# Kernel tuning notes

Measured on AMD Instinct MI355X. Metric: run time of the kernel, lower is better.

The kernel has to match this reference:

```python
import jax, jax.numpy as jnp
import numpy as np

IN_FEATURES = 100000
OUT_FEATURES = 100000
NNZ = 1600000
BATCH = 64


def setup_inputs() -> dict:
    key = jax.random.key(0)
    k1, k2, k3, k4, k5 = jax.random.split(key, 5)
    x = jax.random.normal(k1, (BATCH, IN_FEATURES), dtype=jnp.float32)
    values = jax.random.normal(k2, (NNZ,), dtype=jnp.float32)
    bias = jax.random.normal(k3, (OUT_FEATURES,), dtype=jnp.float32)
    # torch COO is coalesced -> row indices sorted (rows = dst of transposed matrix)
    rows = jnp.sort(jax.random.randint(k4, (NNZ,), 0, OUT_FEATURES, dtype=jnp.int64))
    cols = jax.random.randint(k5, (NNZ,), 0, IN_FEATURES, dtype=jnp.int64)
    return {"x": x, "values": values, "bias": bias, "rows": rows, "cols": cols}


def reference(x, values, bias, rows, cols):
    # out = x @ conn  <=>  out.T = conn_T @ x.T, conn_T given in COO (rows=dst, cols=src)
    # gather source activations along edges: (nnz, B)
    contrib = x[:, cols].T * values[:, None]
    # scatter-add into destinations: (out_features, B)
    out_t = jax.ops.segment_sum(contrib, rows, num_segments=OUT_FEATURES,
                                indices_are_sorted=True)
    return out_t.T + bias  # (B, out_features)
```

## Files before the change

### kernel.cpp

```cpp
#include <hip/hip_runtime.h>
#include <hip/hip_fp16.h>

#define IN_F   100000
#define OUT_F  100000
#define NNZ_N  1600000
#define TC     256
#define TBLK   ((IN_F + TC - 1) / TC)
#define SBLK   ((NNZ_N + 255) / 256)

__device__ __forceinline__ float2 h2f(unsigned u) {
    const __half2 h = *reinterpret_cast<const __half2*>(&u);
    return __half22float2(h);
}

__global__ __launch_bounds__(256) void k_prep(
    const float* __restrict__ x,
    const int*   __restrict__ rows,
    const int*   __restrict__ cols,
    const float* __restrict__ vals,
    unsigned* __restrict__ xh,
    int*      __restrict__ rstart,
    uint2*    __restrict__ pairs) {
    __shared__ unsigned tile[TC][33];
    const int bid = blockIdx.x;
    const int t   = threadIdx.x;

    if (bid < TBLK) {
        const int i0   = bid * TC;
        const int colr = i0 + t;
        if (colr < IN_F) {
            #pragma unroll 8
            for (int p = 0; p < 32; ++p) {
                const float a = x[(size_t)(2 * p)     * IN_F + colr];
                const float b = x[(size_t)(2 * p + 1) * IN_F + colr];
                const __half2 h = __floats2half2_rn(a, b);
                tile[t][p] = *reinterpret_cast<const unsigned*>(&h);
            }
        }
        __syncthreads();
        const int u  = t & 31;
        const int c8 = t >> 5;
        for (int cc = c8; cc < TC; cc += 8) {
            const int col = i0 + cc;
            if (col < IN_F)
                xh[(size_t)col * 32 + u] = tile[cc][u];
        }
    } else {
        const int e = (bid - TBLK) * 256 + t;
        if (e >= NNZ_N) return;
        const int cur  = rows[e];
        const int prev = (e == 0) ? -1 : rows[e - 1];
        for (int r = prev + 1; r <= cur; ++r) rstart[r] = e;
        if (e == NNZ_N - 1)
            for (int r = cur + 1; r <= OUT_F; ++r) rstart[r] = NNZ_N;
        pairs[e] = make_uint2((unsigned)cols[e], __float_as_uint(vals[e]));
    }
}

__global__ __launch_bounds__(512, 4) void k_spmm(
    const uint4* __restrict__ xh4,
    const uint2* __restrict__ pairs,
    const int*   __restrict__ rstart_g,
    const float* __restrict__ bias,
    float* __restrict__ out) {
    __shared__ int   rs[65];
    __shared__ float tile[64][65];
    const int r0   = blockIdx.x * 64;
    const int t    = threadIdx.x;
    const int lane = t & 63;
    const int w    = t >> 6;

    if (t < 65) {
        int idx = r0 + t; if (idx > OUT_F) idx = OUT_F;
        rs[t] = rstart_g[idx];
    }
    __syncthreads();

    const int g   = lane >> 3;
    const int sub = lane & 7;
    const int lj  = (w << 3) + g;
    const int s   = rs[lj];
    const int e   = rs[lj + 1];

    float acc[8];
    #pragma unroll
    for (int i = 0; i < 8; ++i) acc[i] = 0.f;

    for (int base = s; base < e; base += 4) {
        const int e1 = e - 1;
        const int i1 = (base + 1 < e) ? base + 1 : e1;
        const int i2 = (base + 2 < e) ? base + 2 : e1;
        const int i3 = (base + 3 < e) ? base + 3 : e1;
        const uint2 p0 = pairs[base];
        const uint2 p1 = pairs[i1];
        const uint2 p2 = pairs[i2];
        const uint2 p3 = pairs[i3];
        const float v0 = __uint_as_float(p0.y);
        const float v1 = (base + 1 < e) ? __uint_as_float(p1.y) : 0.f;
        const float v2 = (base + 2 < e) ? __uint_as_float(p2.y) : 0.f;
        const float v3 = (base + 3 < e) ? __uint_as_float(p3.y) : 0.f;
        const uint4 u0 = xh4[(size_t)p0.x * 8 + sub];
        const uint4 u1 = xh4[(size_t)p1.x * 8 + sub];
        const uint4 u2 = xh4[(size_t)p2.x * 8 + sub];
        const uint4 u3 = xh4[(size_t)p3.x * 8 + sub];
        float2 f;
        f = h2f(u0.x); acc[0] = fmaf(v0, f.x, acc[0]); acc[1] = fmaf(v0, f.y, acc[1]);
        f = h2f(u0.y); acc[2] = fmaf(v0, f.x, acc[2]); acc[3] = fmaf(v0, f.y, acc[3]);
        f = h2f(u0.z); acc[4] = fmaf(v0, f.x, acc[4]); acc[5] = fmaf(v0, f.y, acc[5]);
        f = h2f(u0.w); acc[6] = fmaf(v0, f.x, acc[6]); acc[7] = fmaf(v0, f.y, acc[7]);
        f = h2f(u1.x); acc[0] = fmaf(v1, f.x, acc[0]); acc[1] = fmaf(v1, f.y, acc[1]);
        f = h2f(u1.y); acc[2] = fmaf(v1, f.x, acc[2]); acc[3] = fmaf(v1, f.y, acc[3]);
        f = h2f(u1.z); acc[4] = fmaf(v1, f.x, acc[4]); acc[5] = fmaf(v1, f.y, acc[5]);
        f = h2f(u1.w); acc[6] = fmaf(v1, f.x, acc[6]); acc[7] = fmaf(v1, f.y, acc[7]);
        f = h2f(u2.x); acc[0] = fmaf(v2, f.x, acc[0]); acc[1] = fmaf(v2, f.y, acc[1]);
        f = h2f(u2.y); acc[2] = fmaf(v2, f.x, acc[2]); acc[3] = fmaf(v2, f.y, acc[3]);
        f = h2f(u2.z); acc[4] = fmaf(v2, f.x, acc[4]); acc[5] = fmaf(v2, f.y, acc[5]);
        f = h2f(u2.w); acc[6] = fmaf(v2, f.x, acc[6]); acc[7] = fmaf(v2, f.y, acc[7]);
        f = h2f(u3.x); acc[0] = fmaf(v3, f.x, acc[0]); acc[1] = fmaf(v3, f.y, acc[1]);
        f = h2f(u3.y); acc[2] = fmaf(v3, f.x, acc[2]); acc[3] = fmaf(v3, f.y, acc[3]);
        f = h2f(u3.z); acc[4] = fmaf(v3, f.x, acc[4]); acc[5] = fmaf(v3, f.y, acc[5]);
        f = h2f(u3.w); acc[6] = fmaf(v3, f.x, acc[6]); acc[7] = fmaf(v3, f.y, acc[7]);
    }

    #pragma unroll
    for (int i = 0; i < 8; ++i) tile[lj][(sub << 3) + i] = acc[i];
    __syncthreads();

    const int rc = r0 + lane;
    if (rc < OUT_F) {
        const float bv = bias[rc];
        for (int bb = w; bb < 64; bb += 8)
            out[(size_t)bb * OUT_F + rc] = tile[lane][bb] + bv;
    }
}

__global__ __launch_bounds__(256) void k_spmm_fallback(
    const float* __restrict__ x,
    const float* __restrict__ vals,
    const int*   __restrict__ rows,
    const int*   __restrict__ cols,
    const float* __restrict__ bias,
    float* __restrict__ out) {
    __shared__ int   rstart[65];
    __shared__ float tile[64][65];
    const int r0   = blockIdx.x * 64;
    const int t    = threadIdx.x;
    const int lane = t & 63;
    const int w    = t >> 6;
    if (t < 65) {
        const int target = r0 + t;
        int lo = 0, hi = NNZ_N;
        while (lo < hi) {
            const int mid = (lo + hi) >> 1;
            if (rows[mid] < target) lo = mid + 1; else hi = mid;
        }
        rstart[t] = lo;
    }
    __syncthreads();
    for (int j = w; j < 64; j += 4) {
        const int s = rstart[j], e = rstart[j + 1];
        float acc = 0.f;
        const size_t base = (size_t)lane * IN_F;
        for (int idx = s; idx < e; ++idx)
            acc = fmaf(vals[idx], x[base + cols[idx]], acc);
        tile[j][lane] = acc;
    }
    __syncthreads();
    const int c = lane;
    if (r0 + c < OUT_F) {
        const float bv = bias[r0 + c];
        for (int bb = w; bb < 64; bb += 4)
            out[(size_t)bb * OUT_F + (r0 + c)] = tile[c][bb] + bv;
    }
}

extern "C" void kernel_launch(void* const* d_in, const int* in_sizes, int n_in,
                              void* d_out, int out_size, void* d_ws, size_t ws_size,
                              hipStream_t stream) {
    const float* x      = (const float*)d_in[0];
    const float* values = (const float*)d_in[1];
    const float* bias   = (const float*)d_in[2];
    const int*   rows   = (const int*)d_in[3];
    const int*   cols   = (const int*)d_in[4];
    float*       out    = (float*)d_out;

    const size_t xh_bytes = (size_t)IN_F * 32 * sizeof(unsigned);
    const size_t rs_off   = (xh_bytes + 255) & ~(size_t)255;
    const size_t rs_bytes = (size_t)(OUT_F + 1) * sizeof(int);
    const size_t pr_off   = (rs_off + rs_bytes + 255) & ~(size_t)255;
    const size_t need     = pr_off + (size_t)NNZ_N * sizeof(uint2);

    const int row_blocks = (OUT_F + 63) / 64;

    if (ws_size >= need) {
        unsigned* xh     = (unsigned*)d_ws;
        int*      rstart = (int*)((char*)d_ws + rs_off);
        uint2*    pairs  = (uint2*)((char*)d_ws + pr_off);
        k_prep<<<TBLK + SBLK, 256, 0, stream>>>(x, rows, cols, values, xh, rstart, pairs);
        k_spmm<<<row_blocks, 512, 0, stream>>>(
            (const uint4*)xh, pairs, rstart, bias, out);
    } else {
        k_spmm_fallback<<<row_blocks, 256, 0, stream>>>(x, values, rows, cols, bias, out);
    }
}
```

Baseline: 132.6 us.

## Bin nonzeros by column chunk per row block to improve gather cache locality

```diff
diff --git a/kernel.cpp b/kernel.cpp
--- a/kernel.cpp
+++ b/kernel.cpp
@@ -6,7 +6,9 @@
 #define NNZ_N  1600000
 #define TC     256
 #define TBLK   ((IN_F + TC - 1) / TC)
-#define SBLK   ((NNZ_N + 255) / 256)
+#define RBLK   ((OUT_F + 63) / 64)
+#define NCH    4
+#define CHW    25000
 
 __device__ __forceinline__ float2 h2f(unsigned u) {
     const __half2 h = *reinterpret_cast<const __half2*>(&u);
@@ -19,9 +21,12 @@
     const int*   __restrict__ cols,
     const float* __restrict__ vals,
     unsigned* __restrict__ xh,
-    int*      __restrict__ rstart,
-    uint2*    __restrict__ pairs) {
+    uint2*    __restrict__ pairs,
+    int*      __restrict__ cs) {
     __shared__ unsigned tile[TC][33];
+    __shared__ int hist[256];
+    __shared__ int off[256];
+    __shared__ int sb[2];
     const int bid = blockIdx.x;
     const int t   = threadIdx.x;
 
@@ -46,87 +51,121 @@
                 xh[(size_t)col * 32 + u] = tile[cc][u];
         }
     } else {
-        const int e = (bid - TBLK) * 256 + t;
-        if (e >= NNZ_N) return;
-        const int cur  = rows[e];
-        const int prev = (e == 0) ? -1 : rows[e - 1];
-        for (int r = prev + 1; r <= cur; ++r) rstart[r] = e;
-        if (e == NNZ_N - 1)
-            for (int r = cur + 1; r <= OUT_F; ++r) rstart[r] = NNZ_N;
-        pairs[e] = make_uint2((unsigned)cols[e], __float_as_uint(vals[e]));
+        const int b  = bid - TBLK;
+        const int r0 = b * 64;
+        if (t < 2) {
+            const int target = r0 + t * 64;
+            int lo = 0, hi = NNZ_N;
+            while (lo < hi) {
+                const int mid = (lo + hi) >> 1;
+                if (rows[mid] < target) lo = mid + 1; else hi = mid;
+            }
+            sb[t] = lo;
+        }
+        hist[t] = 0;
+        __syncthreads();
+        const int s = sb[0], e = sb[1];
+        for (int i = s + t; i < e; i += 256)
+            atomicAdd(&hist[(cols[i] / CHW) * 64 + (rows[i] - r0)], 1);
+        __syncthreads();
+        if (t < 64) {
+            const int s0 = hist[4 * t + 0];
+            const int s1 = hist[4 * t + 1];
+            const int s2 = hist[4 * t + 2];
+            const int s3 = hist[4 * t + 3];
+            const int tot = s0 + s1 + s2 + s3;
+            int sc = tot;
+            #pragma unroll
+            for (int d = 1; d < 64; d <<= 1) {
+                const int n = __shfl_up(sc, d);
+                if (t >= d) sc += n;
+            }
+            int base = s + (sc - tot);
+            off[4 * t + 0] = base; cs[(size_t)b * 257 + 4 * t + 0] = base; base += s0;
+            off[4 * t + 1] = base; cs[(size_t)b * 257 + 4 * t + 1] = base; base += s1;
+            off[4 * t + 2] = base; cs[(size_t)b * 257 + 4 * t + 2] = base; base += s2;
+            off[4 * t + 3] = base; cs[(size_t)b * 257 + 4 * t + 3] = base; base += s3;
+        }
+        if (t == 0) cs[(size_t)b * 257 + 256] = e;
+        __syncthreads();
+        for (int i = s + t; i < e; i += 256) {
+            const int c   = cols[i];
+            const int bin = (c / CHW) * 64 + (rows[i] - r0);
+            const int pos = atomicAdd(&off[bin], 1);
+            pairs[pos] = make_uint2((unsigned)c, __float_as_uint(vals[i]));
+        }
     }
 }
 
 __global__ __launch_bounds__(512, 4) void k_spmm(
     const uint4* __restrict__ xh4,
     const uint2* __restrict__ pairs,
-    const int*   __restrict__ rstart_g,
+    const int*   __restrict__ cs,
     const float* __restrict__ bias,
     float* __restrict__ out) {
-    __shared__ int   rs[65];
+    __shared__ int   rs[257];
     __shared__ float tile[64][65];
-    const int r0   = blockIdx.x * 64;
+    const int b    = blockIdx.x;
     const int t    = threadIdx.x;
     const int lane = t & 63;
     const int w    = t >> 6;
-
-    if (t < 65) {
-        int idx = r0 + t; if (idx > OUT_F) idx = OUT_F;
-        rs[t] = rstart_g[idx];
-    }
-    __syncthreads();
-
-    const int g   = lane >> 3;
-    const int sub = lane & 7;
-    const int lj  = (w << 3) + g;
-    const int s   = rs[lj];
-    const int e   = rs[lj + 1];
+    const int g    = t >> 3;
+    const int sub  = t & 7;
+
+    if (t < 257) rs[t] = cs[(size_t)b * 257 + t];
+    __syncthreads();
 
     float acc[8];
     #pragma unroll
     for (int i = 0; i < 8; ++i) acc[i] = 0.f;
 
-    for (int base = s; base < e; base += 4) {
-        const int e1 = e - 1;
-        const int i1 = (base + 1 < e) ? base + 1 : e1;
-        const int i2 = (base + 2 < e) ? base + 2 : e1;
-        const int i3 = (base + 3 < e) ? base + 3 : e1;
-        const uint2 p0 = pairs[base];
-        const uint2 p1 = pairs[i1];
-        const uint2 p2 = pairs[i2];
-        const uint2 p3 = pairs[i3];
-        const float v0 = __uint_as_float(p0.y);
-        const float v1 = (base + 1 < e) ? __uint_as_float(p1.y) : 0.f;
-        const float v2 = (base + 2 < e) ? __uint_as_float(p2.y) : 0.f;
-        const float v3 = (base + 3 < e) ? __uint_as_float(p3.y) : 0.f;
-        const uint4 u0 = xh4[(size_t)p0.x * 8 + sub];
-        const uint4 u1 = xh4[(size_t)p1.x * 8 + sub];
-        const uint4 u2 = xh4[(size_t)p2.x * 8 + sub];
-        const uint4 u3 = xh4[(size_t)p3.x * 8 + sub];
-        float2 f;
-        f = h2f(u0.x); acc[0] = fmaf(v0, f.x, acc[0]); acc[1] = fmaf(v0, f.y, acc[1]);
-        f = h2f(u0.y); acc[2] = fmaf(v0, f.x, acc[2]); acc[3] = fmaf(v0, f.y, acc[3]);
-        f = h2f(u0.z); acc[4] = fmaf(v0, f.x, acc[4]); acc[5] = fmaf(v0, f.y, acc[5]);
-        f = h2f(u0.w); acc[6] = fmaf(v0, f.x, acc[6]); acc[7] = fmaf(v0, f.y, acc[7]);
-        f = h2f(u1.x); acc[0] = fmaf(v1, f.x, acc[0]); acc[1] = fmaf(v1, f.y, acc[1]);
-        f = h2f(u1.y); acc[2] = fmaf(v1, f.x, acc[2]); acc[3] = fmaf(v1, f.y, acc[3]);
-        f = h2f(u1.z); acc[4] = fmaf(v1, f.x, acc[4]); acc[5] = fmaf(v1, f.y, acc[5]);
-        f = h2f(u1.w); acc[6] = fmaf(v1, f.x, acc[6]); acc[7] = fmaf(v1, f.y, acc[7]);
-        f = h2f(u2.x); acc[0] = fmaf(v2, f.x, acc[0]); acc[1] = fmaf(v2, f.y, acc[1]);
-        f = h2f(u2.y); acc[2] = fmaf(v2, f.x, acc[2]); acc[3] = fmaf(v2, f.y, acc[3]);
-        f = h2f(u2.z); acc[4] = fmaf(v2, f.x, acc[4]); acc[5] = fmaf(v2, f.y, acc[5]);
-        f = h2f(u2.w); acc[6] = fmaf(v2, f.x, acc[6]); acc[7] = fmaf(v2, f.y, acc[7]);
-        f = h2f(u3.x); acc[0] = fmaf(v3, f.x, acc[0]); acc[1] = fmaf(v3, f.y, acc[1]);
-        f = h2f(u3.y); acc[2] = fmaf(v3, f.x, acc[2]); acc[3] = fmaf(v3, f.y, acc[3]);
-        f = h2f(u3.z); acc[4] = fmaf(v3, f.x, acc[4]); acc[5] = fmaf(v3, f.y, acc[5]);
-        f = h2f(u3.w); acc[6] = fmaf(v3, f.x, acc[6]); acc[7] = fmaf(v3, f.y, acc[7]);
-    }
-
     #pragma unroll
-    for (int i = 0; i < 8; ++i) tile[lj][(sub << 3) + i] = acc[i];
-    __syncthreads();
-
-    const int rc = r0 + lane;
+    for (int k = 0; k < NCH; ++k) {
+        const int s = rs[k * 64 + g];
+        const int e = rs[k * 64 + g + 1];
+        for (int base = s; base < e; base += 4) {
+            const int e1 = e - 1;
+            const int i1 = (base + 1 < e) ? base + 1 : e1;
+            const int i2 = (base + 2 < e) ? base + 2 : e1;
+            const int i3 = (base + 3 < e) ? base + 3 : e1;
+            const uint2 p0 = pairs[base];
+            const uint2 p1 = pairs[i1];
+            const uint2 p2 = pairs[i2];
+            const uint2 p3 = pairs[i3];
+            const float v0 = __uint_as_float(p0.y);
+            const float v1 = (base + 1 < e) ? __uint_as_float(p1.y) : 0.f;
+            const float v2 = (base + 2 < e) ? __uint_as_float(p2.y) : 0.f;
+            const float v3 = (base + 3 < e) ? __uint_as_float(p3.y) : 0.f;
+            const uint4 u0 = xh4[(size_t)p0.x * 8 + sub];
+            const uint4 u1 = xh4[(size_t)p1.x * 8 + sub];
+            const uint4 u2 = xh4[(size_t)p2.x * 8 + sub];
+            const uint4 u3 = xh4[(size_t)p3.x * 8 + sub];
+            float2 f;
+            f = h2f(u0.x); acc[0] = fmaf(v0, f.x, acc[0]); acc[1] = fmaf(v0, f.y, acc[1]);
+            f = h2f(u0.y); acc[2] = fmaf(v0, f.x, acc[2]); acc[3] = fmaf(v0, f.y, acc[3]);
+            f = h2f(u0.z); acc[4] = fmaf(v0, f.x, acc[4]); acc[5] = fmaf(v0, f.y, acc[5]);
+            f = h2f(u0.w); acc[6] = fmaf(v0, f.x, acc[6]); acc[7] = fmaf(v0, f.y, acc[7]);
+            f = h2f(u1.x); acc[0] = fmaf(v1, f.x, acc[0]); acc[1] = fmaf(v1, f.y, acc[1]);
+            f = h2f(u1.y); acc[2] = fmaf(v1, f.x, acc[2]); acc[3] = fmaf(v1, f.y, acc[3]);
+            f = h2f(u1.z); acc[4] = fmaf(v1, f.x, acc[4]); acc[5] = fmaf(v1, f.y, acc[5]);
+            f = h2f(u1.w); acc[6] = fmaf(v1, f.x, acc[6]); acc[7] = fmaf(v1, f.y, acc[7]);
+            f = h2f(u2.x); acc[0] = fmaf(v2, f.x, acc[0]); acc[1] = fmaf(v2, f.y, acc[1]);
+            f = h2f(u2.y); acc[2] = fmaf(v2, f.x, acc[2]); acc[3] = fmaf(v2, f.y, acc[3]);
+            f = h2f(u2.z); acc[4] = fmaf(v2, f.x, acc[4]); acc[5] = fmaf(v2, f.y, acc[5]);
+            f = h2f(u2.w); acc[6] = fmaf(v2, f.x, acc[6]); acc[7] = fmaf(v2, f.y, acc[7]);
+            f = h2f(u3.x); acc[0] = fmaf(v3, f.x, acc[0]); acc[1] = fmaf(v3, f.y, acc[1]);
+            f = h2f(u3.y); acc[2] = fmaf(v3, f.x, acc[2]); acc[3] = fmaf(v3, f.y, acc[3]);
+            f = h2f(u3.z); acc[4] = fmaf(v3, f.x, acc[4]); acc[5] = fmaf(v3, f.y, acc[5]);
+            f = h2f(u3.w); acc[6] = fmaf(v3, f.x, acc[6]); acc[7] = fmaf(v3, f.y, acc[7]);
+        }
+        __syncthreads();
+    }
+
+    #pragma unroll
+    for (int i = 0; i < 8; ++i) tile[g][(sub << 3) + i] = acc[i];
+    __syncthreads();
+
+    const int rc = b * 64 + lane;
     if (rc < OUT_F) {
         const float bv = bias[rc];
         for (int bb = w; bb < 64; bb += 8)
@@ -185,21 +224,18 @@
     float*       out    = (float*)d_out;
 
     const size_t xh_bytes = (size_t)IN_F * 32 * sizeof(unsigned);
-    const size_t rs_off   = (xh_bytes + 255) & ~(size_t)255;
-    const size_t rs_bytes = (size_t)(OUT_F + 1) * sizeof(int);
-    const size_t pr_off   = (rs_off + rs_bytes + 255) & ~(size_t)255;
-    const size_t need     = pr_off + (size_t)NNZ_N * sizeof(uint2);
-
-    const int row_blocks = (OUT_F + 63) / 64;
+    const size_t pr_off   = (xh_bytes + 255) & ~(size_t)255;
+    const size_t pr_bytes = (size_t)NNZ_N * sizeof(uint2);
+    const size_t cb_off   = (pr_off + pr_bytes + 255) & ~(size_t)255;
+    const size_t need     = cb_off + (size_t)RBLK * 257 * sizeof(int);
 
     if (ws_size >= need) {
-        unsigned* xh     = (unsigned*)d_ws;
-        int*      rstart = (int*)((char*)d_ws + rs_off);
-        uint2*    pairs  = (uint2*)((char*)d_ws + pr_off);
-        k_prep<<<TBLK + SBLK, 256, 0, stream>>>(x, rows, cols, values, xh, rstart, pairs);
-        k_spmm<<<row_blocks, 512, 0, stream>>>(
-            (const uint4*)xh, pairs, rstart, bias, out);
+        unsigned* xh    = (unsigned*)d_ws;
+        uint2*    pairs = (uint2*)((char*)d_ws + pr_off);
+        int*      cs    = (int*)((char*)d_ws + cb_off);
+        k_prep<<<TBLK + RBLK, 256, 0, stream>>>(x, rows, cols, values, xh, pairs, cs);
+        k_spmm<<<RBLK, 512, 0, stream>>>((const uint4*)xh, pairs, cs, bias, out);
     } else {
-        k_spmm_fallback<<<row_blocks, 256, 0, stream>>>(x, values, rows, cols, bias, out);
-    }
-}
+        k_spmm_fallback<<<RBLK, 256, 0, stream>>>(x, values, rows, cols, bias, out);
+    }
+}
```

After: 149.1 us. +12.5%, slower.

## Drop pairs/rstart preprocessing; binary-search row starts and read cols/vals directly

Applied to the files above, without the earlier changes.

```diff
diff --git a/kernel.cpp b/kernel.cpp
--- a/kernel.cpp
+++ b/kernel.cpp
@@ -6,61 +6,44 @@
 #define NNZ_N  1600000
 #define TC     256
 #define TBLK   ((IN_F + TC - 1) / TC)
-#define SBLK   ((NNZ_N + 255) / 256)
+#define RBLK   ((OUT_F + 63) / 64)
 
 __device__ __forceinline__ float2 h2f(unsigned u) {
     const __half2 h = *reinterpret_cast<const __half2*>(&u);
     return __half22float2(h);
 }
 
-__global__ __launch_bounds__(256) void k_prep(
+__global__ __launch_bounds__(256) void k_transpose(
     const float* __restrict__ x,
-    const int*   __restrict__ rows,
-    const int*   __restrict__ cols,
-    const float* __restrict__ vals,
-    unsigned* __restrict__ xh,
-    int*      __restrict__ rstart,
-    uint2*    __restrict__ pairs) {
+    unsigned*    __restrict__ xh) {
     __shared__ unsigned tile[TC][33];
-    const int bid = blockIdx.x;
-    const int t   = threadIdx.x;
-
-    if (bid < TBLK) {
-        const int i0   = bid * TC;
-        const int colr = i0 + t;
-        if (colr < IN_F) {
-            #pragma unroll 8
-            for (int p = 0; p < 32; ++p) {
-                const float a = x[(size_t)(2 * p)     * IN_F + colr];
-                const float b = x[(size_t)(2 * p + 1) * IN_F + colr];
-                const __half2 h = __floats2half2_rn(a, b);
-                tile[t][p] = *reinterpret_cast<const unsigned*>(&h);
-            }
+    const int i0   = blockIdx.x * TC;
+    const int t    = threadIdx.x;
+    const int colr = i0 + t;
+    if (colr < IN_F) {
+        #pragma unroll 8
+        for (int p = 0; p < 32; ++p) {
+            const float a = x[(size_t)(2 * p)     * IN_F + colr];
+            const float b = x[(size_t)(2 * p + 1) * IN_F + colr];
+            const __half2 h = __floats2half2_rn(a, b);
+            tile[t][p] = *reinterpret_cast<const unsigned*>(&h);
         }
-        __syncthreads();
-        const int u  = t & 31;
-        const int c8 = t >> 5;
-        for (int cc = c8; cc < TC; cc += 8) {
-            const int col = i0 + cc;
-            if (col < IN_F)
-                xh[(size_t)col * 32 + u] = tile[cc][u];
-        }
-    } else {
-        const int e = (bid - TBLK) * 256 + t;
-        if (e >= NNZ_N) return;
-        const int cur  = rows[e];
-        const int prev = (e == 0) ? -1 : rows[e - 1];
-        for (int r = prev + 1; r <= cur; ++r) rstart[r] = e;
-        if (e == NNZ_N - 1)
-            for (int r = cur + 1; r <= OUT_F; ++r) rstart[r] = NNZ_N;
-        pairs[e] = make_uint2((unsigned)cols[e], __float_as_uint(vals[e]));
+    }
+    __syncthreads();
+    const int u  = t & 31;
+    const int c8 = t >> 5;
+    for (int cc = c8; cc < TC; cc += 8) {
+        const int col = i0 + cc;
+        if (col < IN_F)
+            xh[(size_t)col * 32 + u] = tile[cc][u];
     }
 }
 
 __global__ __launch_bounds__(512, 4) void k_spmm(
     const uint4* __restrict__ xh4,
-    const uint2* __restrict__ pairs,
-    const int*   __restrict__ rstart_g,
+    const int*   __restrict__ rows,
+    const int*   __restrict__ cols,
+    const float* __restrict__ vals,
     const float* __restrict__ bias,
     float* __restrict__ out) {
     __shared__ int   rs[65];
@@ -71,8 +54,13 @@
     const int w    = t >> 6;
 
     if (t < 65) {
-        int idx = r0 + t; if (idx > OUT_F) idx = OUT_F;
-        rs[t] = rstart_g[idx];
+        const int target = r0 + t;
+        int lo = 0, hi = NNZ_N;
+        while (lo < hi) {
+            const int mid = (lo + hi) >> 1;
+            if (rows[mid] < target) lo = mid + 1; else hi = mid;
+        }
+        rs[t] = lo;
     }
     __syncthreads();
 
@@ -88,21 +76,19 @@
 
     for (int base = s; base < e; base += 4) {
         const int e1 = e - 1;
-        const int i1 = (base + 1 < e) ? base + 1 : e1;
-        const int i2 = (base + 2 < e) ? base + 2 : e1;
-        const int i3 = (base + 3 < e) ? base + 3 : e1;
-        const uint2 p0 = pairs[base];
-        const uint2 p1 = pairs[i1];
-        const uint2 p2 = pairs[i2];
-        const uint2 p3 = pairs[i3];
-        const float v0 = __uint_as_float(p0.y);
-        const float v1 = (base + 1 < e) ? __uint_as_float(p1.y) : 0.f;
-        const float v2 = (base + 2 < e) ? __uint_as_float(p2.y) : 0.f;
-        const float v3 = (base + 3 < e) ? __uint_as_float(p3.y) : 0.f;
-        const uint4 u0 = xh4[(size_t)p0.x * 8 + sub];
-        const uint4 u1 = xh4[(size_t)p1.x * 8 + sub];
-        const uint4 u2 = xh4[(size_t)p2.x * 8 + sub];
-        const uint4 u3 = xh4[(size_t)p3.x * 8 + sub];
+        const bool m1 = base + 1 < e, m2 = base + 2 < e, m3 = base + 3 < e;
+        const int i1 = m1 ? base + 1 : e1;
+        const int i2 = m2 ? base + 2 : e1;
+        const int i3 = m3 ? base + 3 : e1;
+        const int c0 = cols[base], c1 = cols[i1], c2 = cols[i2], c3 = cols[i3];
+        const float v0 = vals[base];
+        const float v1 = m1 ? vals[i1] : 0.f;
+        const float v2 = m2 ? vals[i2] : 0.f;
+        const float v3 = m3 ? vals[i3] : 0.f;
+        const uint4 u0 = xh4[(size_t)c0 * 8 + sub];
+        const uint4 u1 = xh4[(size_t)c1 * 8 + sub];
+        const uint4 u2 = xh4[(size_t)c2 * 8 + sub];
+        const uint4 u3 = xh4[(size_t)c3 * 8 + sub];
         float2 f;
         f = h2f(u0.x); acc[0] = fmaf(v0, f.x, acc[0]); acc[1] = fmaf(v0, f.y, acc[1]);
         f = h2f(u0.y); acc[2] = fmaf(v0, f.x, acc[2]); acc[3] = fmaf(v0, f.y, acc[3]);
@@ -184,22 +170,13 @@
     const int*   cols   = (const int*)d_in[4];
     float*       out    = (float*)d_out;
 
-    const size_t xh_bytes = (size_t)IN_F * 32 * sizeof(unsigned);
-    const size_t rs_off   = (xh_bytes + 255) & ~(size_t)255;
-    const size_t rs_bytes = (size_t)(OUT_F + 1) * sizeof(int);
-    const size_t pr_off   = (rs_off + rs_bytes + 255) & ~(size_t)255;
-    const size_t need     = pr_off + (size_t)NNZ_N * sizeof(uint2);
-
-    const int row_blocks = (OUT_F + 63) / 64;
+    const size_t need = (size_t)IN_F * 32 * sizeof(unsigned);
 
     if (ws_size >= need) {
-        unsigned* xh     = (unsigned*)d_ws;
-        int*      rstart = (int*)((char*)d_ws + rs_off);
-        uint2*    pairs  = (uint2*)((char*)d_ws + pr_off);
-        k_prep<<<TBLK + SBLK, 256, 0, stream>>>(x, rows, cols, values, xh, rstart, pairs);
-        k_spmm<<<row_blocks, 512, 0, stream>>>(
-            (const uint4*)xh, pairs, rstart, bias, out);
+        unsigned* xh = (unsigned*)d_ws;
+        k_transpose<<<TBLK, 256, 0, stream>>>(x, xh);
+        k_spmm<<<RBLK, 512, 0, stream>>>((const uint4*)xh, rows, cols, values, bias, out);
     } else {
-        k_spmm_fallback<<<row_blocks, 256, 0, stream>>>(x, values, rows, cols, bias, out);
+        k_spmm_fallback<<<RBLK, 256, 0, stream>>>(x, values, rows, cols, bias, out);
     }
 }
```

Measured after the change: 136.2 us. +2.8%, slower.

## Load-balance SpMM over fixed nonzero chunks with shared-memory atomics, drop pairs buffer

Applied to the files above, without the earlier changes.

```diff
diff --git a/kernel.cpp b/kernel.cpp
--- a/kernel.cpp
+++ b/kernel.cpp
@@ -7,6 +7,8 @@
 #define TC     256
 #define TBLK   ((IN_F + TC - 1) / TC)
 #define SBLK   ((NNZ_N + 255) / 256)
+#define RBLK   ((OUT_F + 63) / 64)
+#define CHK    8
 
 __device__ __forceinline__ float2 h2f(unsigned u) {
     const __half2 h = *reinterpret_cast<const __half2*>(&u);
@@ -16,11 +18,8 @@
 __global__ __launch_bounds__(256) void k_prep(
     const float* __restrict__ x,
     const int*   __restrict__ rows,
-    const int*   __restrict__ cols,
-    const float* __restrict__ vals,
     unsigned* __restrict__ xh,
-    int*      __restrict__ rstart,
-    uint2*    __restrict__ pairs) {
+    int*      __restrict__ rstart) {
     __shared__ unsigned tile[TC][33];
     const int bid = blockIdx.x;
     const int t   = threadIdx.x;
@@ -53,17 +52,18 @@
         for (int r = prev + 1; r <= cur; ++r) rstart[r] = e;
         if (e == NNZ_N - 1)
             for (int r = cur + 1; r <= OUT_F; ++r) rstart[r] = NNZ_N;
-        pairs[e] = make_uint2((unsigned)cols[e], __float_as_uint(vals[e]));
     }
 }
 
 __global__ __launch_bounds__(512, 4) void k_spmm(
     const uint4* __restrict__ xh4,
-    const uint2* __restrict__ pairs,
-    const int*   __restrict__ rstart_g,
+    const int*   __restrict__ rstart,
+    const int*   __restrict__ cols,
+    const float* __restrict__ vals,
     const float* __restrict__ bias,
     float* __restrict__ out) {
     __shared__ int   rs[65];
+    __shared__ int   cs[65];
     __shared__ float tile[64][65];
     const int r0   = blockIdx.x * 64;
     const int t    = threadIdx.x;
@@ -72,58 +72,68 @@
 
     if (t < 65) {
         int idx = r0 + t; if (idx > OUT_F) idx = OUT_F;
-        rs[t] = rstart_g[idx];
-    }
-    __syncthreads();
-
-    const int g   = lane >> 3;
-    const int sub = lane & 7;
-    const int lj  = (w << 3) + g;
-    const int s   = rs[lj];
-    const int e   = rs[lj + 1];
-
-    float acc[8];
-    #pragma unroll
-    for (int i = 0; i < 8; ++i) acc[i] = 0.f;
-
-    for (int base = s; base < e; base += 4) {
-        const int e1 = e - 1;
-        const int i1 = (base + 1 < e) ? base + 1 : e1;
-        const int i2 = (base + 2 < e) ? base + 2 : e1;
-        const int i3 = (base + 3 < e) ? base + 3 : e1;
-        const uint2 p0 = pairs[base];
-        const uint2 p1 = pairs[i1];
-        const uint2 p2 = pairs[i2];
-        const uint2 p3 = pairs[i3];
-        const float v0 = __uint_as_float(p0.y);
-        const float v1 = (base + 1 < e) ? __uint_as_float(p1.y) : 0.f;
-        const float v2 = (base + 2 < e) ? __uint_as_float(p2.y) : 0.f;
-        const float v3 = (base + 3 < e) ? __uint_as_float(p3.y) : 0.f;
-        const uint4 u0 = xh4[(size_t)p0.x * 8 + sub];
-        const uint4 u1 = xh4[(size_t)p1.x * 8 + sub];
-        const uint4 u2 = xh4[(size_t)p2.x * 8 + sub];
-        const uint4 u3 = xh4[(size_t)p3.x * 8 + sub];
-        float2 f;
-        f = h2f(u0.x); acc[0] = fmaf(v0, f.x, acc[0]); acc[1] = fmaf(v0, f.y, acc[1]);
-        f = h2f(u0.y); acc[2] = fmaf(v0, f.x, acc[2]); acc[3] = fmaf(v0, f.y, acc[3]);
-        f = h2f(u0.z); acc[4] = fmaf(v0, f.x, acc[4]); acc[5] = fmaf(v0, f.y, acc[5]);
-        f = h2f(u0.w); acc[6] = fmaf(v0, f.x, acc[6]); acc[7] = fmaf(v0, f.y, acc[7]);
-        f = h2f(u1.x); acc[0] = fmaf(v1, f.x, acc[0]); acc[1] = fmaf(v1, f.y, acc[1]);
-        f = h2f(u1.y); acc[2] = fmaf(v1, f.x, acc[2]); acc[3] = fmaf(v1, f.y, acc[3]);
-        f = h2f(u1.z); acc[4] = fmaf(v1, f.x, acc[4]); acc[5] = fmaf(v1, f.y, acc[5]);
-        f = h2f(u1.w); acc[6] = fmaf(v1, f.x, acc[6]); acc[7] = fmaf(v1, f.y, acc[7]);
-        f = h2f(u2.x); acc[0] = fmaf(v2, f.x, acc[0]); acc[1] = fmaf(v2, f.y, acc[1]);
-        f = h2f(u2.y); acc[2] = fmaf(v2, f.x, acc[2]); acc[3] = fmaf(v2, f.y, acc[3]);
-        f = h2f(u2.z); acc[4] = fmaf(v2, f.x, acc[4]); acc[5] = fmaf(v2, f.y, acc[5]);
-        f = h2f(u2.w); acc[6] = fmaf(v2, f.x, acc[6]); acc[7] = fmaf(v2, f.y, acc[7]);
-        f = h2f(u3.x); acc[0] = fmaf(v3, f.x, acc[0]); acc[1] = fmaf(v3, f.y, acc[1]);
-        f = h2f(u3.y); acc[2] = fmaf(v3, f.x, acc[2]); acc[3] = fmaf(v3, f.y, acc[3]);
-        f = h2f(u3.z); acc[4] = fmaf(v3, f.x, acc[4]); acc[5] = fmaf(v3, f.y, acc[5]);
-        f = h2f(u3.w); acc[6] = fmaf(v3, f.x, acc[6]); acc[7] = fmaf(v3, f.y, acc[7]);
-    }
-
-    #pragma unroll
-    for (int i = 0; i < 8; ++i) tile[lj][(sub << 3) + i] = acc[i];
+        rs[t] = rstart[idx];
+    }
+    float* tp = &tile[0][0];
+    for (int i = t; i < 64 * 65; i += 512) tp[i] = 0.f;
+    __syncthreads();
+
+    if (t < 64) {
+        const int n = (rs[t + 1] - rs[t] + CHK - 1) / CHK;
+        int sc = n;
+        #pragma unroll
+        for (int d = 1; d < 64; d <<= 1) {
+            const int nb = __shfl_up(sc, d);
+            if (t >= d) sc += nb;
+        }
+        cs[t + 1] = sc;
+        if (t == 0) cs[0] = 0;
+    }
+    __syncthreads();
+
+    const int NC  = cs[64];
+    const int gg  = t >> 3;
+    const int sub = t & 7;
+
+    for (int k = gg; k < NC; k += 64) {
+        int lo = 0, hi = 64;
+        #pragma unroll
+        for (int it = 0; it < 6; ++it) {
+            const int mid = (lo + hi) >> 1;
+            if (cs[mid] <= k) lo = mid; else hi = mid;
+        }
+        const int r  = lo;
+        const int b0 = rs[r] + (k - cs[r]) * CHK;
+        const int bn = rs[r + 1];
+        const int b1 = (b0 + CHK < bn) ? b0 + CHK : bn;
+
+        int   c[CHK]; float v[CHK];
+        #pragma unroll
+        for (int j = 0; j < CHK; ++j) {
+            const int i = (b0 + j < b1) ? b0 + j : b1 - 1;
+            c[j] = cols[i];
+            v[j] = (b0 + j < b1) ? vals[i] : 0.f;
+        }
+        uint4 u[CHK];
+        #pragma unroll
+        for (int j = 0; j < CHK; ++j)
+            u[j] = xh4[(size_t)c[j] * 8 + sub];
+
+        float acc[8];
+        #pragma unroll
+        for (int i = 0; i < 8; ++i) acc[i] = 0.f;
+        #pragma unroll
+        for (int j = 0; j < CHK; ++j) {
+            float2 f;
+            f = h2f(u[j].x); acc[0] = fmaf(v[j], f.x, acc[0]); acc[1] = fmaf(v[j], f.y, acc[1]);
+            f = h2f(u[j].y); acc[2] = fmaf(v[j], f.x, acc[2]); acc[3] = fmaf(v[j], f.y, acc[3]);
+            f = h2f(u[j].z); acc[4] = fmaf(v[j], f.x, acc[4]); acc[5] = fmaf(v[j], f.y, acc[5]);
+            f = h2f(u[j].w); acc[6] = fmaf(v[j], f.x, acc[6]); acc[7] = fmaf(v[j], f.y, acc[7]);
+        }
+        #pragma unroll
+        for (int i = 0; i < 8; ++i)
+            atomicAdd(&tile[r][(sub << 3) + i], acc[i]);
+    }
     __syncthreads();
 
     const int rc = r0 + lane;
@@ -186,20 +196,14 @@
 
     const size_t xh_bytes = (size_t)IN_F * 32 * sizeof(unsigned);
     const size_t rs_off   = (xh_bytes + 255) & ~(size_t)255;
-    const size_t rs_bytes = (size_t)(OUT_F + 1) * sizeof(int);
-    const size_t pr_off   = (rs_off + rs_bytes + 255) & ~(size_t)255;
-    const size_t need     = pr_off + (size_t)NNZ_N * sizeof(uint2);
-
-    const int row_blocks = (OUT_F + 63) / 64;
+    const size_t need     = rs_off + (size_t)(OUT_F + 1) * sizeof(int);
 
     if (ws_size >= need) {
         unsigned* xh     = (unsigned*)d_ws;
         int*      rstart = (int*)((char*)d_ws + rs_off);
-        uint2*    pairs  = (uint2*)((char*)d_ws + pr_off);
-        k_prep<<<TBLK + SBLK, 256, 0, stream>>>(x, rows, cols, values, xh, rstart, pairs);
-        k_spmm<<<row_blocks, 512, 0, stream>>>(
-            (const uint4*)xh, pairs, rstart, bias, out);
+        k_prep<<<TBLK + SBLK, 256, 0, stream>>>(x, rows, xh, rstart);
+        k_spmm<<<RBLK, 512, 0, stream>>>((const uint4*)xh, rstart, cols, values, bias, out);
     } else {
-        k_spmm_fallback<<<row_blocks, 256, 0, stream>>>(x, values, rows, cols, bias, out);
-    }
-}
+        k_spmm_fallback<<<RBLK, 256, 0, stream>>>(x, values, rows, cols, bias, out);
+    }
+}
```

Measured after the change: 193.9 us. 46.3% more time.
